# Kernel optimization log

Hardware: AMD Instinct MI355X
Metric: run time of the kernel (lower is better)

The kernel has to match this reference:

```python
import jax, jax.numpy as jnp
import numpy as np

H, C = 8, 32          # heads, out_channels per head (H*C = 256)
D = H * C
NEG_SLOPE = 0.2
SELF_LOOP_TYPE = 6    # num_edge_types - 1
EPS_LN = 1e-5
EPS_BN = 1e-5


def _gat_layer(x, src, dst, ea, et, Ws, Wd, a_s, a_d, We, ae, te, Wo, bo, b, lg, lb):
    N = x.shape[0]
    xs = (x @ Ws).reshape(N, H, C)   # lin_src -> x_j features
    xd = (x @ Wd).reshape(N, H, C)   # lin_dst -> x_i features
    # per-node attention logits (gathered per edge): alpha = <x_i, att_src> + <x_j, att_dst>
    a_i = jnp.einsum('nhc,hc->nh', xd, a_s)  # paired with x_i (dst)
    a_j = jnp.einsum('nhc,hc->nh', xs, a_d)  # paired with x_j (src)
    alpha = a_i[dst] + a_j[src]                                  # [E, H]
    ef = (ea @ We).reshape(-1, H, C)                              # lin_edge
    alpha = alpha + jnp.einsum('ehc,hc->eh', ef, ae)
    tf = te[et].reshape(-1, H, C)                                 # edge_type_emb
    alpha = alpha + jnp.einsum('ehc,hc->eh', tf, ae)
    alpha = jnp.where(alpha >= 0, alpha, NEG_SLOPE * alpha)       # leaky_relu
    # segment softmax over destination nodes (every node has a self loop)
    m = jax.ops.segment_max(alpha, dst, num_segments=N)
    e = jnp.exp(alpha - m[dst])
    s = jax.ops.segment_sum(e, dst, num_segments=N)
    alpha = e / (s[dst] + 1e-16)                                  # [E, H]
    # dropout is identity in eval mode
    msg = xs[src] * alpha[:, :, None]                             # [E, H, C]
    out = jax.ops.segment_sum(msg, dst, num_segments=N).reshape(N, D)
    out = out @ Wo + bo + b                                       # lin_out + bias
    mu = out.mean(-1, keepdims=True)
    var = out.var(-1, keepdims=True)
    out = (out - mu) / jnp.sqrt(var + EPS_LN) * lg + lb           # layer norm
    return out + x                                                # in_channels == H*C residual


def _bn_relu(x, g, bvec, relu=True):
    mu = x.mean(0)
    var = x.var(0)
    x = (x - mu) / jnp.sqrt(var + EPS_BN) * g + bvec
    return jnp.maximum(x, 0.0) if relu else x


def _forward(x, edge_index, edge_attr, edge_types,
             Ws1, Wd1, as1, ad1, We1, ae1, te1, Wo1, bo1, b1, lg1, lb1,
             Ws2, Wd2, as2, ad2, We2, ae2, te2, Wo2, bo2, b2, lg2, lb2,
             bng1, bnb1, bng2, bnb2):
    N = x.shape[0]
    loops = jnp.arange(N, dtype=edge_index.dtype)
    src = jnp.concatenate([edge_index[0], loops])
    dst = jnp.concatenate([edge_index[1], loops])
    ea = jnp.concatenate([edge_attr, jnp.ones((N, edge_attr.shape[1]), edge_attr.dtype)])
    et = jnp.concatenate([edge_types, jnp.full((N,), SELF_LOOP_TYPE, edge_types.dtype)])
    residual = x  # in_channels == out_channels -> identity projection
    out = _gat_layer(x, src, dst, ea, et, Ws1, Wd1, as1, ad1, We1, ae1, te1, Wo1, bo1, b1, lg1, lb1)
    out = _bn_relu(out, bng1, bnb1, relu=True)   # dropout identity in eval
    out = _gat_layer(out, src, dst, ea, et, Ws2, Wd2, as2, ad2, We2, ae2, te2, Wo2, bo2, b2, lg2, lb2)
    out = _bn_relu(out, bng2, bnb2, relu=False)
    return jnp.maximum(out + residual, 0.0)


def setup_inputs() -> dict:
    key = jax.random.key(0)
    ks = jax.random.split(key, 32)
    N, E, EDIM, NTYPES = 20000, 320000, 16, 7
    d = {}
    d['x'] = jax.random.normal(ks[0], (N, D), jnp.float32)
    d['edge_index'] = jax.random.randint(ks[1], (2, E), 0, N, jnp.int64)
    d['edge_attr'] = jax.random.normal(ks[2], (E, EDIM), jnp.float32)
    d['edge_types'] = jax.random.randint(ks[3], (E,), 0, NTYPES, jnp.int64)
    def glorot(k, shape):
        fan = shape[-2] + shape[-1] if len(shape) >= 2 else shape[-1] + 1
        return jax.random.uniform(k, shape, jnp.float32, -1.0, 1.0) * np.sqrt(6.0 / fan)
    i = 4
    for L in ('1', '2'):
        d['Ws' + L] = glorot(ks[i], (D, D)); i += 1
        d['Wd' + L] = glorot(ks[i], (D, D)); i += 1
        d['as' + L] = glorot(ks[i], (H, C)); i += 1
        d['ad' + L] = glorot(ks[i], (H, C)); i += 1
        d['We' + L] = glorot(ks[i], (EDIM, D)); i += 1
        d['ae' + L] = glorot(ks[i], (H, C)); i += 1
        d['te' + L] = glorot(ks[i], (NTYPES, D)); i += 1
        d['Wo' + L] = glorot(ks[i], (D, D)); i += 1
        d['bo' + L] = jnp.zeros((D,), jnp.float32)
        d['b' + L] = jnp.zeros((D,), jnp.float32)
        d['lg' + L] = jnp.ones((D,), jnp.float32)
        d['lb' + L] = jnp.zeros((D,), jnp.float32)
    d['bng1'] = jnp.ones((D,), jnp.float32); d['bnb1'] = jnp.zeros((D,), jnp.float32)
    d['bng2'] = jnp.ones((D,), jnp.float32); d['bnb2'] = jnp.zeros((D,), jnp.float32)
    return d


def reference(x, edge_index, edge_attr, edge_types,
              Ws1, Wd1, as1, ad1, We1, ae1, te1, Wo1, bo1, b1, lg1, lb1,
              Ws2, Wd2, as2, ad2, We2, ae2, te2, Wo2, bo2, b2, lg2, lb2,
              bng1, bnb1, bng2, bnb2):
    return _forward(x, edge_index, edge_attr, edge_types,
                    Ws1, Wd1, as1, ad1, We1, ae1, te1, Wo1, bo1, b1, lg1, lb1,
                    Ws2, Wd2, as2, ad2, We2, ae2, te2, Wo2, bo2, b2, lg2, lb2,
                    bng1, bnb1, bng2, bnb2)
```

## Files before the change

kernel.cpp:

```cpp
#include <hip/hip_runtime.h>

#define DD 256
#define HH 8
#define CC 32

typedef __attribute__((ext_vector_type(8))) short short8;
typedef __attribute__((ext_vector_type(4))) float f32x4;

static __device__ __forceinline__ unsigned short f2b(float f){
  unsigned u = __float_as_uint(f);
  u = u + 0x7FFFu + ((u >> 16) & 1u);
  return (unsigned short)(u >> 16);
}
static __device__ __forceinline__ float b2f(unsigned short s){
  return __uint_as_float(((unsigned)s) << 16);
}

__global__ void k_zero_i(int* p, int n){ int i=blockIdx.x*blockDim.x+threadIdx.x; if(i<n) p[i]=0; }

__global__ void k_count(const int* __restrict__ dstE, int E, int N, int* cnt){
  int e=blockIdx.x*blockDim.x+threadIdx.x;
  if(e<E+N){ int d=(e<E)? dstE[e] : (e-E); atomicAdd(&cnt[d],1); }
}

__global__ __launch_bounds__(1024) void k_scan(const int* __restrict__ cnt, int N, int* row_off, int* cursor){
  __shared__ int part[1024];
  int t=threadIdx.x;
  int chunk=(N+1023)>>10;
  int s=0;
  for(int j=0;j<chunk;j++){ int i=t*chunk+j; if(i<N) s+=cnt[i]; }
  part[t]=s; __syncthreads();
  for(int off=1; off<1024; off<<=1){
    int v=(t>=off)? part[t-off]:0;
    __syncthreads();
    part[t]+=v;
    __syncthreads();
  }
  int run=(t==0)?0:part[t-1];
  for(int j=0;j<chunk;j++){ int i=t*chunk+j; if(i<N){ row_off[i]=run; cursor[i]=run; run+=cnt[i]; } }
  if(t==1023) row_off[N]=part[1023];
}

__global__ void k_fill(const int* __restrict__ srcE, const int* __restrict__ dstE, int E, int N,
                       int* cursor, int* epos, int* esrc){
  int e=blockIdx.x*blockDim.x+threadIdx.x;
  if(e>=E+N) return;
  int s,d;
  if(e<E){ s=srcE[e]; d=dstE[e]; } else { s=e-E; d=s; }
  int pos=atomicAdd(&cursor[d],1);
  epos[e]=pos; esrc[pos]=s;
}

__global__ void k_cvt_wT4(const float* __restrict__ W0, const float* __restrict__ W1,
                          const float* __restrict__ W2, const float* __restrict__ W3,
                          unsigned short* __restrict__ T0, unsigned short* __restrict__ T1,
                          unsigned short* __restrict__ T2, unsigned short* __restrict__ T3){
  int m=blockIdx.y, c=blockIdx.x, k=threadIdx.x;
  const float* W = (m==0)?W0:(m==1)?W1:(m==2)?W2:W3;
  unsigned short* T = (m==0)?T0:(m==1)?T1:(m==2)?T2:T3;
  T[(size_t)c*DD+k] = f2b(W[(size_t)k*DD+c]);
}

__global__ void k_pre2(const float* __restrict__ Wd1, const float* __restrict__ as1,
                       const float* __restrict__ We1, const float* __restrict__ ae1,
                       const float* __restrict__ te1,
                       const float* __restrict__ Wd2, const float* __restrict__ as2,
                       const float* __restrict__ We2, const float* __restrict__ ae2,
                       const float* __restrict__ te2,
                       float* wd_as1, float* v_e1, float* t_a1,
                       float* wd_as2, float* v_e2, float* t_a2){
  int L=blockIdx.x;
  const float* Wd=L?Wd2:Wd1; const float* as_=L?as2:as1;
  const float* We=L?We2:We1; const float* ae=L?ae2:ae1; const float* te=L?te2:te1;
  float* wd_as=L?wd_as2:wd_as1; float* v_e=L?v_e2:v_e1; float* t_a=L?t_a2:t_a1;
  int t=threadIdx.x;
  for(int idx=t; idx<DD*HH; idx+=256){
    int k=idx>>3, h=idx&7;
    const float* w=&Wd[k*DD+h*CC]; const float* a=&as_[h*CC];
    float s=0;
    #pragma unroll
    for(int c=0;c<CC;c++) s+=w[c]*a[c];
    wd_as[idx]=s;
  }
  for(int idx=t; idx<16*HH; idx+=256){
    int k=idx>>3, h=idx&7;
    const float* w=&We[k*DD+h*CC]; const float* a=&ae[h*CC];
    float s=0;
    #pragma unroll
    for(int c=0;c<CC;c++) s+=w[c]*a[c];
    v_e[idx]=s;
  }
  for(int idx=t; idx<7*HH; idx+=256){
    int k=idx>>3, h=idx&7;
    const float* w=&te[k*DD+h*CC]; const float* a=&ae[h*CC];
    float s=0;
    #pragma unroll
    for(int c=0;c<CC;c++) s+=w[c]*a[c];
    t_a[idx]=s;
  }
}

#define NB_BA 1024
__global__ __launch_bounds__(256) void k_cvt_x2(const float* __restrict__ xin, const float* __restrict__ wd_as,
                         unsigned short* __restrict__ xb, float* __restrict__ a_i, int N){
  int b=blockIdx.x, tid=threadIdx.x, wv=tid>>6, l=tid&63;
  int c0=4*l;
  float wa[4][8];
  #pragma unroll
  for(int j=0;j<4;j++)
    #pragma unroll
    for(int h=0;h<8;h++) wa[j][h]=wd_as[(c0+j)*8+h];
  for(int n=b*4+wv; n<N; n+=NB_BA*4){
    float4 v=*(const float4*)&xin[(size_t)n*DD+c0];
    ushort4 xo; xo.x=f2b(v.x); xo.y=f2b(v.y); xo.z=f2b(v.z); xo.w=f2b(v.w);
    *(ushort4*)&xb[(size_t)n*DD+c0]=xo;
    float ai[8];
    #pragma unroll
    for(int h=0;h<8;h++) ai[h]=v.x*wa[0][h]+v.y*wa[1][h]+v.z*wa[2][h]+v.w*wa[3][h];
    #pragma unroll
    for(int off=1;off<64;off<<=1){
      #pragma unroll
      for(int h=0;h<8;h++) ai[h]+=__shfl_xor(ai[h],off);
    }
    if(l==0){
      float4 A; A.x=ai[0];A.y=ai[1];A.z=ai[2];A.w=ai[3];
      float4 B; B.x=ai[4];B.y=ai[5];B.z=ai[6];B.w=ai[7];
      *(float4*)&a_i[(size_t)n*HH]=A;
      *(float4*)&a_i[(size_t)n*HH+4]=B;
    }
  }
}

template<bool AJ>
__global__ __launch_bounds__(256) void k_gemm1(const unsigned short* __restrict__ A,
                                               const unsigned short* __restrict__ Bt,
                                               const float* __restrict__ ad, float* __restrict__ a_j,
                                               unsigned short* __restrict__ Cout, int N){
  __shared__ char lds[4096 + 8192];
  int tid=threadIdx.x;
  int w=tid>>6, l=tid&63;
  int row0=blockIdx.y*64, col0=blockIdx.x*128;

  int sr=tid>>2, skc=tid&3;
  int kcs=skc^((sr>>1)&3);
  int aslot=sr*4+skc;
  int bslot1=sr*4+skc, bslot2=(sr+64)*4+skc;
  int gr=row0+sr;
  size_t boff1=(size_t)(col0+sr)*DD, boff2=(size_t)(col0+64+sr)*DD;

  int x15=l&15;
  int lp=x15*64 + ((l>>4)^((x15>>1)&3))*16;

  f32x4 acc[4][2];
  #pragma unroll
  for(int i=0;i<4;i++){ acc[i][0]=(f32x4)0.f; acc[i][1]=(f32x4)0.f; }

  const short8 zero8=(short8)0;
  short8 av,bv1,bv2;
  av  = (gr<N) ? *(const short8*)&A[(size_t)gr*DD + kcs*8] : zero8;
  bv1 = *(const short8*)&Bt[boff1 + kcs*8];
  bv2 = *(const short8*)&Bt[boff2 + kcs*8];

  for(int kt=0;kt<DD;kt+=32){
    __syncthreads();
    *(short8*)(lds + aslot*16) = av;
    *(short8*)(lds + 4096 + bslot1*16) = bv1;
    *(short8*)(lds + 4096 + bslot2*16) = bv2;
    __syncthreads();
    if(kt+32<DD){
      int ko=kt+32+kcs*8;
      av  = (gr<N) ? *(const short8*)&A[(size_t)gr*DD + ko] : zero8;
      bv1 = *(const short8*)&Bt[boff1 + ko];
      bv2 = *(const short8*)&Bt[boff2 + ko];
    }
    short8 af[4], bf[2];
    #pragma unroll
    for(int mf=0;mf<4;mf++) af[mf]=*(short8*)(lds + mf*1024 + lp);
    #pragma unroll
    for(int nf=0;nf<2;nf++) bf[nf]=*(short8*)(lds + 4096 + (32*w+16*nf)*64 + lp);
    #pragma unroll
    for(int mf=0;mf<4;mf++)
      #pragma unroll
      for(int nf=0;nf<2;nf++)
        acc[mf][nf]=__builtin_amdgcn_mfma_f32_16x16x32_bf16(af[mf],bf[nf],acc[mf][nf],0,0,0);
  }

  int lcol=x15, lrow4=(l>>4)*4;
  float ad0=0.f, ad1=0.f;
  if(AJ){ ad0=ad[col0+32*w+lcol]; ad1=ad[col0+32*w+16+lcol]; }
  int head=(col0>>5)+w;
  #pragma unroll
  for(int mf=0;mf<4;mf++){
    #pragma unroll
    for(int nf=0;nf<2;nf++){
      int col=col0 + 32*w + 16*nf + lcol;
      #pragma unroll
      for(int rr=0;rr<4;rr++){
        int row=row0 + 16*mf + lrow4 + rr;
        if(row<N) Cout[(size_t)row*DD+col]=f2b(acc[mf][nf][rr]);
      }
    }
    if(AJ){
      #pragma unroll
      for(int rr=0;rr<4;rr++){
        float t=acc[mf][0][rr]*ad0 + acc[mf][1][rr]*ad1;
        t+=__shfl_xor(t,1); t+=__shfl_xor(t,2);
        t+=__shfl_xor(t,4); t+=__shfl_xor(t,8);
        int row=row0 + 16*mf + lrow4 + rr;
        if(x15==0 && row<N) a_j[(size_t)row*HH+head]=t;
      }
    }
  }
}

__global__ __launch_bounds__(256) void k_gemm_ln(const unsigned short* __restrict__ A,
                                                 const unsigned short* __restrict__ Bt,
                                                 const float* __restrict__ bo, const float* __restrict__ bvec,
                                                 const float* __restrict__ xin,
                                                 const float* __restrict__ lg, const float* __restrict__ lb,
                                                 float* __restrict__ hout,
                                                 float* __restrict__ psum, float* __restrict__ psq, int N){
  __shared__ char lds[2048 + 16384];
  int tid=threadIdx.x;
  int w=tid>>6, l=tid&63;
  int row0=blockIdx.x*32;

  int sr=tid>>2, skc=tid&3;
  int kcs=skc^((sr>>1)&3);
  int aslot=sr*4+skc;
  int gr=row0+sr;
  size_t boff0=(size_t)(sr)*DD, boff1=(size_t)(64+sr)*DD,
         boff2=(size_t)(128+sr)*DD, boff3=(size_t)(192+sr)*DD;
  int bs0=sr*4+skc, bs1=(sr+64)*4+skc, bs2=(sr+128)*4+skc, bs3=(sr+192)*4+skc;

  int x15=l&15;
  int lp=x15*64 + ((l>>4)^((x15>>1)&3))*16;

  f32x4 acc[2][4];
  #pragma unroll
  for(int i=0;i<2;i++)
    #pragma unroll
    for(int j=0;j<4;j++) acc[i][j]=(f32x4)0.f;

  const short8 zero8=(short8)0;
  short8 av=zero8,b0,b1,b2,b3;
  if(tid<128) av = (gr<N) ? *(const short8*)&A[(size_t)gr*DD + kcs*8] : zero8;
  b0=*(const short8*)&Bt[boff0 + kcs*8];
  b1=*(const short8*)&Bt[boff1 + kcs*8];
  b2=*(const short8*)&Bt[boff2 + kcs*8];
  b3=*(const short8*)&Bt[boff3 + kcs*8];

  for(int kt=0;kt<DD;kt+=32){
    __syncthreads();
    if(tid<128) *(short8*)(lds + aslot*16) = av;
    *(short8*)(lds + 2048 + bs0*16) = b0;
    *(short8*)(lds + 2048 + bs1*16) = b1;
    *(short8*)(lds + 2048 + bs2*16) = b2;
    *(short8*)(lds + 2048 + bs3*16) = b3;
    __syncthreads();
    if(kt+32<DD){
      int ko=kt+32+kcs*8;
      if(tid<128) av = (gr<N) ? *(const short8*)&A[(size_t)gr*DD + ko] : zero8;
      b0=*(const short8*)&Bt[boff0 + ko];
      b1=*(const short8*)&Bt[boff1 + ko];
      b2=*(const short8*)&Bt[boff2 + ko];
      b3=*(const short8*)&Bt[boff3 + ko];
    }
    short8 af[2], bf[4];
    #pragma unroll
    for(int mf=0;mf<2;mf++) af[mf]=*(short8*)(lds + mf*1024 + lp);
    #pragma unroll
    for(int nf=0;nf<4;nf++) bf[nf]=*(short8*)(lds + 2048 + w*4096 + nf*1024 + lp);
    #pragma unroll
    for(int mf=0;mf<2;mf++)
      #pragma unroll
      for(int nf=0;nf<4;nf++)
        acc[mf][nf]=__builtin_amdgcn_mfma_f32_16x16x32_bf16(af[mf],bf[nf],acc[mf][nf],0,0,0);
  }

  int lrow4=(l>>4)*4;
  float lgv[4], lbv[4];
  #pragma unroll
  for(int nf=0;nf<4;nf++){
    int col=64*w+16*nf+x15;
    float badd=bo[col]+bvec[col];
    lgv[nf]=lg[col]; lbv[nf]=lb[col];
    #pragma unroll
    for(int mf=0;mf<2;mf++)
      #pragma unroll
      for(int rr=0;rr<4;rr++) acc[mf][nf][rr]+=badd;
  }
  __syncthreads();
  float* rs   =(float*)lds;
  float* rq   =(float*)(lds+512);
  float* mus  =(float*)(lds+1024);
  float* rstds=(float*)(lds+1152);
  #pragma unroll
  for(int mf=0;mf<2;mf++){
    #pragma unroll
    for(int rr=0;rr<4;rr++){
      float t=acc[mf][0][rr]+acc[mf][1][rr]+acc[mf][2][rr]+acc[mf][3][rr];
      float q=acc[mf][0][rr]*acc[mf][0][rr]+acc[mf][1][rr]*acc[mf][1][rr]
             +acc[mf][2][rr]*acc[mf][2][rr]+acc[mf][3][rr]*acc[mf][3][rr];
      t+=__shfl_xor(t,1); q+=__shfl_xor(q,1);
      t+=__shfl_xor(t,2); q+=__shfl_xor(q,2);
      t+=__shfl_xor(t,4); q+=__shfl_xor(q,4);
      t+=__shfl_xor(t,8); q+=__shfl_xor(q,8);
      if(x15==0){
        int row=16*mf+lrow4+rr;
        rs[w*32+row]=t; rq[w*32+row]=q;
      }
    }
  }
  __syncthreads();
  if(tid<32){
    float S=rs[tid]+rs[32+tid]+rs[64+tid]+rs[96+tid];
    float Q=rq[tid]+rq[32+tid]+rq[64+tid]+rq[96+tid];
    float mu=S*(1.f/DD);
    float var=Q*(1.f/DD)-mu*mu;
    mus[tid]=mu;
    rstds[tid]=rsqrtf(var+1e-5f);
  }
  __syncthreads();
  float cps[4]={0.f,0.f,0.f,0.f}, cqs[4]={0.f,0.f,0.f,0.f};
  #pragma unroll
  for(int mf=0;mf<2;mf++){
    #pragma unroll
    for(int rr=0;rr<4;rr++){
      int row=16*mf+lrow4+rr;
      int grow=row0+row;
      bool ok=(grow<N);
      float mu=mus[row], rstd=rstds[row];
      #pragma unroll
      for(int nf=0;nf<4;nf++){
        int col=64*w+16*nf+x15;
        float h=0.f;
        if(ok){
          h=(acc[mf][nf][rr]-mu)*rstd*lgv[nf]+lbv[nf]+xin[(size_t)grow*DD+col];
          hout[(size_t)grow*DD+col]=h;
        }
        cps[nf]+=h; cqs[nf]+=h*h;
      }
    }
  }
  #pragma unroll
  for(int nf=0;nf<4;nf++){
    cps[nf]+=__shfl_xor(cps[nf],16); cqs[nf]+=__shfl_xor(cqs[nf],16);
    cps[nf]+=__shfl_xor(cps[nf],32); cqs[nf]+=__shfl_xor(cqs[nf],32);
  }
  if(l<16){
    #pragma unroll
    for(int nf=0;nf<4;nf++){
      int col=64*w+16*nf+l;
      psum[(size_t)blockIdx.x*DD+col]=cps[nf];
      psq [(size_t)blockIdx.x*DD+col]=cqs[nf];
    }
  }
}

__global__ void k_edge(const int* __restrict__ srcE, const int* __restrict__ dstE,
                       const float* __restrict__ ea, const int* __restrict__ et,
                       const int* __restrict__ epos,
                       const float* __restrict__ a_i, const float* __restrict__ a_j,
                       const float* __restrict__ v_e, const float* __restrict__ t_a,
                       float* __restrict__ alphaP, int E, int N){
  int e=blockIdx.x*blockDim.x+threadIdx.x;
  if(e>=E+N) return;
  int s,d,ty;
  float eattr[16];
  if(e<E){
    s=srcE[e]; d=dstE[e]; ty=et[e];
    float4 q0=*(const float4*)&ea[(size_t)e*16+0];
    float4 q1=*(const float4*)&ea[(size_t)e*16+4];
    float4 q2=*(const float4*)&ea[(size_t)e*16+8];
    float4 q3=*(const float4*)&ea[(size_t)e*16+12];
    eattr[0]=q0.x;eattr[1]=q0.y;eattr[2]=q0.z;eattr[3]=q0.w;
    eattr[4]=q1.x;eattr[5]=q1.y;eattr[6]=q1.z;eattr[7]=q1.w;
    eattr[8]=q2.x;eattr[9]=q2.y;eattr[10]=q2.z;eattr[11]=q2.w;
    eattr[12]=q3.x;eattr[13]=q3.y;eattr[14]=q3.z;eattr[15]=q3.w;
  }else{
    s=e-E; d=s; ty=6;
    #pragma unroll
    for(int k=0;k<16;k++) eattr[k]=1.f;
  }
  int pos=epos[e];
  const float* ai=&a_i[(size_t)d*8];
  const float* aj=&a_j[(size_t)s*8];
  #pragma unroll
  for(int h=0;h<8;h++){
    float v=ai[h]+aj[h]+t_a[ty*8+h];
    #pragma unroll
    for(int k=0;k<16;k++) v+=eattr[k]*v_e[k*8+h];
    alphaP[(size_t)pos*8+h] = (v>=0.f)? v : 0.2f*v;
  }
}

__global__ __launch_bounds__(256) void k_agg(const int* __restrict__ row_off,
                      const int* __restrict__ esrc, const float* __restrict__ alphaP,
                      const unsigned short* __restrict__ ysb, unsigned short* __restrict__ aggb, int N){
  int wv=threadIdx.x>>6, l=threadIdx.x&63;
  int n=blockIdx.x*4+wv;
  if(n>=N) return;
  int beg=row_off[n], deg=row_off[n+1]-beg;
  int slotL=l>>3, headL=l&7;
  float mx=-3e38f;
  for(int i=slotL;i<deg;i+=8) mx=fmaxf(mx, alphaP[(size_t)(beg+i)*8+headL]);
  mx=fmaxf(mx,__shfl_xor(mx,8));
  mx=fmaxf(mx,__shfl_xor(mx,16));
  mx=fmaxf(mx,__shfl_xor(mx,32));
  int ghead=l>>3;
  float ssum=0.f, acc0=0.f, acc1=0.f, acc2=0.f, acc3=0.f;
  float a_c; int s_c;
  {
    int i=slotL; bool ok=(i<deg); int ic=ok?i:(deg-1);
    a_c = ok ? alphaP[(size_t)(beg+i)*8+headL] : -3e38f;
    s_c = esrc[beg+ic];
  }
  for(int base=0;base<deg;base+=8){
    float a_n=-3e38f; int s_n=0;
    if(base+8<deg){
      int i=base+8+slotL; bool ok=(i<deg); int ic=ok?i:(deg-1);
      a_n = ok ? alphaP[(size_t)(beg+i)*8+headL] : -3e38f;
      s_n = esrc[beg+ic];
    }
    float wvv=__expf(a_c-mx);
    int cnt=min(8,deg-base);
    #pragma unroll
    for(int u=0;u<8;u++){
      if(u<cnt){
        float wgt=__shfl(wvv,(u<<3)|ghead);
        int   si =__shfl(s_c,(u<<3));
        ssum+=wgt;
        ushort4 y=*(const ushort4*)&ysb[(size_t)si*DD+4*l];
        acc0+=wgt*b2f(y.x); acc1+=wgt*b2f(y.y); acc2+=wgt*b2f(y.z); acc3+=wgt*b2f(y.w);
      }
    }
    a_c=a_n; s_c=s_n;
  }
  float inv=1.f/(ssum+1e-16f);
  ushort4 o;
  o.x=f2b(acc0*inv); o.y=f2b(acc1*inv); o.z=f2b(acc2*inv); o.w=f2b(acc3*inv);
  *(ushort4*)&aggb[(size_t)n*DD+4*l]=o;
}

__global__ __launch_bounds__(256) void k_bnfin(const float* __restrict__ psum, const float* __restrict__ psq,
                        const float* __restrict__ g, const float* __restrict__ b,
                        float* scale, float* shift, int N, int nb){
  __shared__ float rs[256], rq[256];
  int c=blockIdx.x, tid=threadIdx.x;
  float s=0.f,q=0.f;
  for(int i=tid;i<nb;i+=256){ s+=psum[(size_t)i*DD+c]; q+=psq[(size_t)i*DD+c]; }
  rs[tid]=s; rq[tid]=q;
  __syncthreads();
  #pragma unroll
  for(int off=128;off>0;off>>=1){
    if(tid<off){ rs[tid]+=rs[tid+off]; rq[tid]+=rq[tid+off]; }
    __syncthreads();
  }
  if(tid==0){
    float inv=1.f/(float)N;
    float mu=rs[0]*inv;
    float var=rq[0]*inv - mu*mu;
    float sc=g[c]*rsqrtf(var+1e-5f);
    scale[c]=sc;
    shift[c]=b[c]-mu*sc;
  }
}

template<bool RES, bool CVT>
__global__ __launch_bounds__(256) void k_bnapply(const float* __restrict__ hm, const float* __restrict__ scale,
                          const float* __restrict__ shift, const float* __restrict__ res,
                          float* __restrict__ outp, unsigned short* __restrict__ xb,
                          const float* __restrict__ wd_as, float* __restrict__ a_i, int N){
  int b=blockIdx.x, tid=threadIdx.x, wv=tid>>6, l=tid&63;
  int c0=4*l;
  float4 sc=*(const float4*)&scale[c0];
  float4 sh=*(const float4*)&shift[c0];
  float wa[4][8];
  if(CVT){
    #pragma unroll
    for(int j=0;j<4;j++)
      #pragma unroll
      for(int h=0;h<8;h++) wa[j][h]=wd_as[(c0+j)*8+h];
  }
  for(int n=b*4+wv; n<N; n+=NB_BA*4){
    float4 v=*(const float4*)&hm[(size_t)n*DD+c0];
    v.x=v.x*sc.x+sh.x; v.y=v.y*sc.y+sh.y; v.z=v.z*sc.z+sh.z; v.w=v.w*sc.w+sh.w;
    if(RES){
      float4 rr=*(const float4*)&res[(size_t)n*DD+c0];
      v.x+=rr.x; v.y+=rr.y; v.z+=rr.z; v.w+=rr.w;
    }
    v.x=fmaxf(v.x,0.f); v.y=fmaxf(v.y,0.f); v.z=fmaxf(v.z,0.f); v.w=fmaxf(v.w,0.f);
    *(float4*)&outp[(size_t)n*DD+c0]=v;
    if(CVT){
      ushort4 xo; xo.x=f2b(v.x); xo.y=f2b(v.y); xo.z=f2b(v.z); xo.w=f2b(v.w);
      *(ushort4*)&xb[(size_t)n*DD+c0]=xo;
      float ai[8];
      #pragma unroll
      for(int h=0;h<8;h++) ai[h]=v.x*wa[0][h]+v.y*wa[1][h]+v.z*wa[2][h]+v.w*wa[3][h];
      #pragma unroll
      for(int off=1;off<64;off<<=1){
        #pragma unroll
        for(int h=0;h<8;h++) ai[h]+=__shfl_xor(ai[h],off);
      }
      if(l==0){
        float4 A; A.x=ai[0];A.y=ai[1];A.z=ai[2];A.w=ai[3];
        float4 B; B.x=ai[4];B.y=ai[5];B.z=ai[6];B.w=ai[7];
        *(float4*)&a_i[(size_t)n*HH]=A;
        *(float4*)&a_i[(size_t)n*HH+4]=B;
      }
    }
  }
}

extern "C" void kernel_launch(void* const* d_in, const int* in_sizes, int n_in,
                              void* d_out, int out_size, void* d_ws, size_t ws_size,
                              hipStream_t stream) {
  const float* x  = (const float*)d_in[0];
  const int*   ei = (const int*)d_in[1];
  const float* ea = (const float*)d_in[2];
  const int*   et = (const int*)d_in[3];
  int N = in_sizes[0]/DD;
  int E = in_sizes[3];
  int Etot = E+N;
  const int* srcE = ei;
  const int* dstE = ei + E;

  const float* Ws1=(const float*)d_in[4];  const float* Wd1=(const float*)d_in[5];
  const float* as1=(const float*)d_in[6];  const float* ad1=(const float*)d_in[7];
  const float* We1=(const float*)d_in[8];  const float* ae1=(const float*)d_in[9];
  const float* te1=(const float*)d_in[10]; const float* Wo1=(const float*)d_in[11];
  const float* bo1=(const float*)d_in[12]; const float* b1 =(const float*)d_in[13];
  const float* lg1=(const float*)d_in[14]; const float* lb1=(const float*)d_in[15];
  const float* Ws2=(const float*)d_in[16]; const float* Wd2=(const float*)d_in[17];
  const float* as2=(const float*)d_in[18]; const float* ad2=(const float*)d_in[19];
  const float* We2=(const float*)d_in[20]; const float* ae2=(const float*)d_in[21];
  const float* te2=(const float*)d_in[22]; const float* Wo2=(const float*)d_in[23];
  const float* bo2=(const float*)d_in[24]; const float* b2 =(const float*)d_in[25];
  const float* lg2=(const float*)d_in[26]; const float* lb2=(const float*)d_in[27];
  const float* bng1=(const float*)d_in[28]; const float* bnb1=(const float*)d_in[29];
  const float* bng2=(const float*)d_in[30]; const float* bnb2=(const float*)d_in[31];

  char* p=(char*)d_ws;
  auto alloc=[&](size_t bytes)->void*{ void* r=(void*)p; p+=(bytes+255)&~(size_t)255; return r; };
  unsigned short* xb   =(unsigned short*)alloc((size_t)N*DD*2);
  unsigned short* ysb  =(unsigned short*)alloc((size_t)N*DD*2);
  unsigned short* aggb =(unsigned short*)alloc((size_t)N*DD*2);
  float* alphaP=(float*)alloc((size_t)Etot*HH*4);
  float* xout1 =(float*)alloc((size_t)N*DD*4);
  float* a_i   =(float*)alloc((size_t)N*HH*4);
  float* a_j   =(float*)alloc((size_t)N*HH*4);
  float* wd_as1=(float*)alloc(DD*HH*4);
  float* v_e1  =(float*)alloc(16*HH*4);
  float* t_a1  =(float*)alloc(7*HH*4);
  float* wd_as2=(float*)alloc(DD*HH*4);
  float* v_e2  =(float*)alloc(16*HH*4);
  float* t_a2  =(float*)alloc(7*HH*4);
  int nbLN=(N+31)/32;
  float* psum  =(float*)alloc((size_t)nbLN*DD*4);
  float* psq   =(float*)alloc((size_t)nbLN*DD*4);
  float* scl   =(float*)alloc(256*4);
  float* shf   =(float*)alloc(256*4);
  unsigned short* Wsb1T=(unsigned short*)alloc((size_t)DD*DD*2);
  unsigned short* Wob1T=(unsigned short*)alloc((size_t)DD*DD*2);
  unsigned short* Wsb2T=(unsigned short*)alloc((size_t)DD*DD*2);
  unsigned short* Wob2T=(unsigned short*)alloc((size_t)DD*DD*2);
  int* cnt     =(int*)alloc((size_t)N*4);
  int* row_off =(int*)alloc((size_t)(N+1)*4);
  int* cursor  =(int*)alloc((size_t)N*4);
  int* epos    =(int*)alloc((size_t)Etot*4);
  int* esrc    =(int*)alloc((size_t)Etot*4);
  float* hbuf  =(float*)d_out;

  dim3 gg(2,(N+63)/64);
  int aggGrid=(N+3)/4;

  k_zero_i<<<(N+255)/256,256,0,stream>>>(cnt,N);
  k_count<<<(Etot+255)/256,256,0,stream>>>(dstE,E,N,cnt);
  k_scan<<<1,1024,0,stream>>>(cnt,N,row_off,cursor);
  k_fill<<<(Etot+255)/256,256,0,stream>>>(srcE,dstE,E,N,cursor,epos,esrc);
  k_cvt_wT4<<<dim3(DD,4),DD,0,stream>>>(Ws1,Wo1,Ws2,Wo2,Wsb1T,Wob1T,Wsb2T,Wob2T);
  k_pre2<<<2,256,0,stream>>>(Wd1,as1,We1,ae1,te1,Wd2,as2,We2,ae2,te2,
                             wd_as1,v_e1,t_a1,wd_as2,v_e2,t_a2);

  k_cvt_x2<<<NB_BA,256,0,stream>>>(x,wd_as1,xb,a_i,N);
  k_gemm1<true><<<gg,256,0,stream>>>(xb,Wsb1T,ad1,a_j,ysb,N);
  k_edge<<<(Etot+255)/256,256,0,stream>>>(srcE,dstE,ea,et,epos,a_i,a_j,v_e1,t_a1,alphaP,E,N);
  k_agg<<<aggGrid,256,0,stream>>>(row_off,esrc,alphaP,ysb,aggb,N);
  k_gemm_ln<<<nbLN,256,0,stream>>>(aggb,Wob1T,bo1,b1,x,lg1,lb1,hbuf,psum,psq,N);
  k_bnfin<<<DD,256,0,stream>>>(psum,psq,bng1,bnb1,scl,shf,N,nbLN);
  k_bnapply<false,true><<<NB_BA,256,0,stream>>>(hbuf,scl,shf,nullptr,xout1,xb,wd_as2,a_i,N);

  k_gemm1<true><<<gg,256,0,stream>>>(xb,Wsb2T,ad2,a_j,ysb,N);
  k_edge<<<(Etot+255)/256,256,0,stream>>>(srcE,dstE,ea,et,epos,a_i,a_j,v_e2,t_a2,alphaP,E,N);
  k_agg<<<aggGrid,256,0,stream>>>(row_off,esrc,alphaP,ysb,aggb,N);
  k_gemm_ln<<<nbLN,256,0,stream>>>(aggb,Wob2T,bo2,b2,xout1,lg2,lb2,hbuf,psum,psq,N);
  k_bnfin<<<DD,256,0,stream>>>(psum,psq,bng2,bnb2,scl,shf,N,nbLN);
  k_bnapply<true,false><<<NB_BA,256,0,stream>>>(hbuf,scl,shf,x,(float*)d_out,nullptr,nullptr,nullptr,N);
}
```

Measured before the change: 322.3 us.

## Use async global-to-LDS double buffering in GEMMs and degree-sort nodes for aggregation

Both GEMM kernels now load tiles directly from global memory into LDS with global_load_lds and double-buffer the LDS so the next k-tile streams in while MFMAs run on the current one. A counting sort by in-degree reorders nodes so aggregation waves in a block handle similar-degree nodes, reducing load imbalance. This adds four small setup kernels and an indirection, doubles LDS use per block, and drops the row bounds guard on A loads.

```diff
diff --git a/kernel.cpp b/kernel.cpp
--- a/kernel.cpp
+++ b/kernel.cpp
@@ -14,6 +14,12 @@
 }
 static __device__ __forceinline__ float b2f(unsigned short s){
   return __uint_as_float(((unsigned)s) << 16);
+}
+
+static __device__ __forceinline__ void gload16(const void* g, void* l){
+  using gpt = const __attribute__((address_space(1))) unsigned int*;
+  using lpt = __attribute__((address_space(3))) unsigned int*;
+  __builtin_amdgcn_global_load_lds((gpt)(unsigned long long)g, (lpt)(unsigned long long)l, 16, 0, 0);
 }
 
 __global__ void k_zero_i(int* p, int n){ int i=blockIdx.x*blockDim.x+threadIdx.x; if(i<n) p[i]=0; }
@@ -49,6 +55,27 @@
   if(e<E){ s=srcE[e]; d=dstE[e]; } else { s=e-E; d=s; }
   int pos=atomicAdd(&cursor[d],1);
   epos[e]=pos; esrc[pos]=s;
+}
+
+__global__ void k_hist(const int* __restrict__ cnt, int N, int* bins){
+  int n=blockIdx.x*blockDim.x+threadIdx.x;
+  if(n<N) atomicAdd(&bins[min(cnt[n],1023)],1);
+}
+__global__ __launch_bounds__(1024) void k_scanb(int* bins){
+  __shared__ int part[1024];
+  int t=threadIdx.x;
+  part[t]=bins[t]; __syncthreads();
+  for(int off=1;off<1024;off<<=1){
+    int v=(t>=off)?part[t-off]:0;
+    __syncthreads();
+    part[t]+=v;
+    __syncthreads();
+  }
+  bins[t]=(t==0)?0:part[t-1];
+}
+__global__ void k_scatter(const int* __restrict__ cnt, int N, int* bins, int* nsort){
+  int n=blockIdx.x*blockDim.x+threadIdx.x;
+  if(n<N){ int pos=atomicAdd(&bins[min(cnt[n],1023)],1); nsort[pos]=n; }
 }
 
 __global__ void k_cvt_wT4(const float* __restrict__ W0, const float* __restrict__ W1,
@@ -136,17 +163,19 @@
                                                const unsigned short* __restrict__ Bt,
                                                const float* __restrict__ ad, float* __restrict__ a_j,
                                                unsigned short* __restrict__ Cout, int N){
-  __shared__ char lds[4096 + 8192];
+  __shared__ char lds[2*12288];
   int tid=threadIdx.x;
   int w=tid>>6, l=tid&63;
   int row0=blockIdx.y*64, col0=blockIdx.x*128;
 
-  int sr=tid>>2, skc=tid&3;
-  int kcs=skc^((sr>>1)&3);
-  int aslot=sr*4+skc;
-  int bslot1=sr*4+skc, bslot2=(sr+64)*4+skc;
-  int gr=row0+sr;
-  size_t boff1=(size_t)(col0+sr)*DD, boff2=(size_t)(col0+64+sr)*DD;
+  int lr=l>>2;
+  int kc=(l&3)^((l>>3)&3);
+  const unsigned short* ga  = &A [(size_t)(row0+16*w+lr)*DD + kc*8];
+  const unsigned short* gb0 = &Bt[(size_t)(col0+32*w+lr)*DD + kc*8];
+  const unsigned short* gb1 = &Bt[(size_t)(col0+32*w+16+lr)*DD + kc*8];
+  int laoff =      w*1024;
+  int lboff0=4096+(32*w)*64;
+  int lboff1=4096+(32*w+16)*64;
 
   int x15=l&15;
   int lp=x15*64 + ((l>>4)^((x15>>1)&3))*16;
@@ -155,34 +184,31 @@
   #pragma unroll
   for(int i=0;i<4;i++){ acc[i][0]=(f32x4)0.f; acc[i][1]=(f32x4)0.f; }
 
-  const short8 zero8=(short8)0;
-  short8 av,bv1,bv2;
-  av  = (gr<N) ? *(const short8*)&A[(size_t)gr*DD + kcs*8] : zero8;
-  bv1 = *(const short8*)&Bt[boff1 + kcs*8];
-  bv2 = *(const short8*)&Bt[boff2 + kcs*8];
-
+  gload16(ga,  lds+laoff);
+  gload16(gb0, lds+lboff0);
+  gload16(gb1, lds+lboff1);
+  __syncthreads();
+  int cur=0;
   for(int kt=0;kt<DD;kt+=32){
-    __syncthreads();
-    *(short8*)(lds + aslot*16) = av;
-    *(short8*)(lds + 4096 + bslot1*16) = bv1;
-    *(short8*)(lds + 4096 + bslot2*16) = bv2;
-    __syncthreads();
+    int nxt=cur^1;
     if(kt+32<DD){
-      int ko=kt+32+kcs*8;
-      av  = (gr<N) ? *(const short8*)&A[(size_t)gr*DD + ko] : zero8;
-      bv1 = *(const short8*)&Bt[boff1 + ko];
-      bv2 = *(const short8*)&Bt[boff2 + ko];
-    }
+      gload16(ga +kt+32, lds+nxt*12288+laoff);
+      gload16(gb0+kt+32, lds+nxt*12288+lboff0);
+      gload16(gb1+kt+32, lds+nxt*12288+lboff1);
+    }
+    char* base=lds+cur*12288;
     short8 af[4], bf[2];
     #pragma unroll
-    for(int mf=0;mf<4;mf++) af[mf]=*(short8*)(lds + mf*1024 + lp);
-    #pragma unroll
-    for(int nf=0;nf<2;nf++) bf[nf]=*(short8*)(lds + 4096 + (32*w+16*nf)*64 + lp);
+    for(int mf=0;mf<4;mf++) af[mf]=*(short8*)(base + mf*1024 + lp);
+    #pragma unroll
+    for(int nf=0;nf<2;nf++) bf[nf]=*(short8*)(base + 4096 + (32*w+16*nf)*64 + lp);
     #pragma unroll
     for(int mf=0;mf<4;mf++)
       #pragma unroll
       for(int nf=0;nf<2;nf++)
         acc[mf][nf]=__builtin_amdgcn_mfma_f32_16x16x32_bf16(af[mf],bf[nf],acc[mf][nf],0,0,0);
+    __syncthreads();
+    cur=nxt;
   }
 
   int lcol=x15, lrow4=(l>>4)*4;
@@ -220,18 +246,23 @@
                                                  const float* __restrict__ lg, const float* __restrict__ lb,
                                                  float* __restrict__ hout,
                                                  float* __restrict__ psum, float* __restrict__ psq, int N){
-  __shared__ char lds[2048 + 16384];
+  __shared__ char lds[2*18432];
   int tid=threadIdx.x;
   int w=tid>>6, l=tid&63;
   int row0=blockIdx.x*32;
 
-  int sr=tid>>2, skc=tid&3;
-  int kcs=skc^((sr>>1)&3);
-  int aslot=sr*4+skc;
-  int gr=row0+sr;
-  size_t boff0=(size_t)(sr)*DD, boff1=(size_t)(64+sr)*DD,
-         boff2=(size_t)(128+sr)*DD, boff3=(size_t)(192+sr)*DD;
-  int bs0=sr*4+skc, bs1=(sr+64)*4+skc, bs2=(sr+128)*4+skc, bs3=(sr+192)*4+skc;
+  int lr=l>>2;
+  int kc=(l&3)^((l>>3)&3);
+  const unsigned short* ga = &A[(size_t)(row0+16*w+lr)*DD + kc*8];
+  const unsigned short* gb0=&Bt[(size_t)(64*w   +lr)*DD + kc*8];
+  const unsigned short* gb1=&Bt[(size_t)(64*w+16+lr)*DD + kc*8];
+  const unsigned short* gb2=&Bt[(size_t)(64*w+32+lr)*DD + kc*8];
+  const unsigned short* gb3=&Bt[(size_t)(64*w+48+lr)*DD + kc*8];
+  int laoff =      w*1024;
+  int lboff0=2048+(64*w   )*64;
+  int lboff1=2048+(64*w+16)*64;
+  int lboff2=2048+(64*w+32)*64;
+  int lboff3=2048+(64*w+48)*64;
 
   int x15=l&15;
   int lp=x15*64 + ((l>>4)^((x15>>1)&3))*16;
@@ -242,40 +273,36 @@
     #pragma unroll
     for(int j=0;j<4;j++) acc[i][j]=(f32x4)0.f;
 
-  const short8 zero8=(short8)0;
-  short8 av=zero8,b0,b1,b2,b3;
-  if(tid<128) av = (gr<N) ? *(const short8*)&A[(size_t)gr*DD + kcs*8] : zero8;
-  b0=*(const short8*)&Bt[boff0 + kcs*8];
-  b1=*(const short8*)&Bt[boff1 + kcs*8];
-  b2=*(const short8*)&Bt[boff2 + kcs*8];
-  b3=*(const short8*)&Bt[boff3 + kcs*8];
-
+  if(w<2) gload16(ga, lds+laoff);
+  gload16(gb0, lds+lboff0);
+  gload16(gb1, lds+lboff1);
+  gload16(gb2, lds+lboff2);
+  gload16(gb3, lds+lboff3);
+  __syncthreads();
+  int cur=0;
   for(int kt=0;kt<DD;kt+=32){
-    __syncthreads();
-    if(tid<128) *(short8*)(lds + aslot*16) = av;
-    *(short8*)(lds + 2048 + bs0*16) = b0;
-    *(short8*)(lds + 2048 + bs1*16) = b1;
-    *(short8*)(lds + 2048 + bs2*16) = b2;
-    *(short8*)(lds + 2048 + bs3*16) = b3;
-    __syncthreads();
+    int nxt=cur^1;
     if(kt+32<DD){
-      int ko=kt+32+kcs*8;
-      if(tid<128) av = (gr<N) ? *(const short8*)&A[(size_t)gr*DD + ko] : zero8;
-      b0=*(const short8*)&Bt[boff0 + ko];
-      b1=*(const short8*)&Bt[boff1 + ko];
-      b2=*(const short8*)&Bt[boff2 + ko];
-      b3=*(const short8*)&Bt[boff3 + ko];
-    }
+      char* nb=lds+nxt*18432;
+      if(w<2) gload16(ga+kt+32, nb+laoff);
+      gload16(gb0+kt+32, nb+lboff0);
+      gload16(gb1+kt+32, nb+lboff1);
+      gload16(gb2+kt+32, nb+lboff2);
+      gload16(gb3+kt+32, nb+lboff3);
+    }
+    char* base=lds+cur*18432;
     short8 af[2], bf[4];
     #pragma unroll
-    for(int mf=0;mf<2;mf++) af[mf]=*(short8*)(lds + mf*1024 + lp);
-    #pragma unroll
-    for(int nf=0;nf<4;nf++) bf[nf]=*(short8*)(lds + 2048 + w*4096 + nf*1024 + lp);
+    for(int mf=0;mf<2;mf++) af[mf]=*(short8*)(base + mf*1024 + lp);
+    #pragma unroll
+    for(int nf=0;nf<4;nf++) bf[nf]=*(short8*)(base + 2048 + (64*w+16*nf)*64 + lp);
     #pragma unroll
     for(int mf=0;mf<2;mf++)
       #pragma unroll
       for(int nf=0;nf<4;nf++)
         acc[mf][nf]=__builtin_amdgcn_mfma_f32_16x16x32_bf16(af[mf],bf[nf],acc[mf][nf],0,0,0);
+    __syncthreads();
+    cur=nxt;
   }
 
   int lrow4=(l>>4)*4;
@@ -395,12 +422,13 @@
   }
 }
 
-__global__ __launch_bounds__(256) void k_agg(const int* __restrict__ row_off,
+__global__ __launch_bounds__(256) void k_agg(const int* __restrict__ row_off, const int* __restrict__ nsort,
                       const int* __restrict__ esrc, const float* __restrict__ alphaP,
                       const unsigned short* __restrict__ ysb, unsigned short* __restrict__ aggb, int N){
   int wv=threadIdx.x>>6, l=threadIdx.x&63;
-  int n=blockIdx.x*4+wv;
-  if(n>=N) return;
+  int idx=blockIdx.x*4+wv;
+  if(idx>=N) return;
+  int n=nsort[idx];
   int beg=row_off[n], deg=row_off[n+1]-beg;
   int slotL=l>>3, headL=l&7;
   float mx=-3e38f;
@@ -570,6 +598,8 @@
   int* cursor  =(int*)alloc((size_t)N*4);
   int* epos    =(int*)alloc((size_t)Etot*4);
   int* esrc    =(int*)alloc((size_t)Etot*4);
+  int* bins    =(int*)alloc(1024*4);
+  int* nsort   =(int*)alloc((size_t)N*4);
   float* hbuf  =(float*)d_out;
 
   dim3 gg(2,(N+63)/64);
@@ -579,6 +609,10 @@
   k_count<<<(Etot+255)/256,256,0,stream>>>(dstE,E,N,cnt);
   k_scan<<<1,1024,0,stream>>>(cnt,N,row_off,cursor);
   k_fill<<<(Etot+255)/256,256,0,stream>>>(srcE,dstE,E,N,cursor,epos,esrc);
+  k_zero_i<<<4,256,0,stream>>>(bins,1024);
+  k_hist<<<(N+255)/256,256,0,stream>>>(cnt,N,bins);
+  k_scanb<<<1,1024,0,stream>>>(bins);
+  k_scatter<<<(N+255)/256,256,0,stream>>>(cnt,N,bins,nsort);
   k_cvt_wT4<<<dim3(DD,4),DD,0,stream>>>(Ws1,Wo1,Ws2,Wo2,Wsb1T,Wob1T,Wsb2T,Wob2T);
   k_pre2<<<2,256,0,stream>>>(Wd1,as1,We1,ae1,te1,Wd2,as2,We2,ae2,te2,
                              wd_as1,v_e1,t_a1,wd_as2,v_e2,t_a2);
@@ -586,14 +620,14 @@
   k_cvt_x2<<<NB_BA,256,0,stream>>>(x,wd_as1,xb,a_i,N);
   k_gemm1<true><<<gg,256,0,stream>>>(xb,Wsb1T,ad1,a_j,ysb,N);
   k_edge<<<(Etot+255)/256,256,0,stream>>>(srcE,dstE,ea,et,epos,a_i,a_j,v_e1,t_a1,alphaP,E,N);
-  k_agg<<<aggGrid,256,0,stream>>>(row_off,esrc,alphaP,ysb,aggb,N);
+  k_agg<<<aggGrid,256,0,stream>>>(row_off,nsort,esrc,alphaP,ysb,aggb,N);
   k_gemm_ln<<<nbLN,256,0,stream>>>(aggb,Wob1T,bo1,b1,x,lg1,lb1,hbuf,psum,psq,N);
   k_bnfin<<<DD,256,0,stream>>>(psum,psq,bng1,bnb1,scl,shf,N,nbLN);
   k_bnapply<false,true><<<NB_BA,256,0,stream>>>(hbuf,scl,shf,nullptr,xout1,xb,wd_as2,a_i,N);
 
   k_gemm1<true><<<gg,256,0,stream>>>(xb,Wsb2T,ad2,a_j,ysb,N);
   k_edge<<<(Etot+255)/256,256,0,stream>>>(srcE,dstE,ea,et,epos,a_i,a_j,v_e2,t_a2,alphaP,E,N);
-  k_agg<<<aggGrid,256,0,stream>>>(row_off,esrc,alphaP,ysb,aggb,N);
+  k_agg<<<aggGrid,256,0,stream>>>(row_off,nsort,esrc,alphaP,ysb,aggb,N);
   k_gemm_ln<<<nbLN,256,0,stream>>>(aggb,Wob2T,bo2,b2,xout1,lg2,lb2,hbuf,psum,psq,N);
   k_bnfin<<<DD,256,0,stream>>>(psum,psq,bng2,bnb2,scl,shf,N,nbLN);
   k_bnapply<true,false><<<NB_BA,256,0,stream>>>(hbuf,scl,shf,x,(float*)d_out,nullptr,nullptr,nullptr,N);
```

Measured after the change: 436.7 us. 35.5% more time.
